# Performance work log

Measured on AMD Instinct MI355X. Metric: run time of the kernel, lower is better.

Reference implementation:

```python
import jax, jax.numpy as jnp
import numpy as np

N, IN_DIM, HID, OUT = 100000, 256, 256, 128
E = 500000


def setup_inputs() -> dict:
    key = jax.random.key(0)
    ks = jax.random.split(key, 12)
    s_in = 1.0 / np.sqrt(IN_DIM)
    s_h = 1.0 / np.sqrt(HID)
    s_c = 1.0 / np.sqrt(2 * OUT)
    return {
        "x": jax.random.normal(ks[0], (N, IN_DIM), dtype=jnp.float32),
        "pos_u": jax.random.randint(ks[1], (E,), 0, N),
        "pos_v": jax.random.randint(ks[2], (E,), 0, N),
        "neg_u": jax.random.randint(ks[3], (E,), 0, N),
        "neg_v": jax.random.randint(ks[4], (E,), 0, N),
        "Wn1": jax.random.normal(ks[5], (IN_DIM, HID), dtype=jnp.float32) * s_in,
        "bn1": jnp.zeros((HID,), dtype=jnp.float32),
        "Wn2": jax.random.normal(ks[6], (HID, OUT), dtype=jnp.float32) * s_h,
        "bn2": jnp.zeros((OUT,), dtype=jnp.float32),
        "Ws1": jax.random.normal(ks[7], (2 * OUT, HID), dtype=jnp.float32) * s_c,
        "bs1": jnp.zeros((HID,), dtype=jnp.float32),
        "Ws2": jax.random.normal(ks[8], (HID, 1), dtype=jnp.float32) * s_h,
        "bs2": jnp.zeros((1,), dtype=jnp.float32),
    }


def _pair_logits(H, u, v, Ws1, bs1, Ws2, bs2):
    hu = H[u]  # [E, OUT] gather
    hv = H[v]
    feats = jnp.concatenate([jnp.abs(hu - hv), hu * hv], axis=-1)  # [E, 2*OUT]
    h = jax.nn.relu(feats @ Ws1 + bs1)
    return (h @ Ws2 + bs2)[..., 0]  # [E]


def reference(x, pos_u, pos_v, neg_u, neg_v,
              Wn1, bn1, Wn2, bn2, Ws1, bs1, Ws2, bs2):
    # node encoder MLP (dropout = identity in eval)
    H = jax.nn.relu(x @ Wn1 + bn1) @ Wn2 + bn2  # [N, OUT]
    pos_logit = _pair_logits(H, pos_u, pos_v, Ws1, bs1, Ws2, bs2)
    neg_logit = _pair_logits(H, neg_u, neg_v, Ws1, bs1, Ws2, bs2)
    return (pos_logit, neg_logit, H)
```

## Files before the change

kernel.cpp:

```cpp
#include <hip/hip_runtime.h>

typedef unsigned short u16;
typedef __bf16 bf16x8 __attribute__((ext_vector_type(8)));
typedef float f32x4 __attribute__((ext_vector_type(4)));
typedef unsigned int u32x4 __attribute__((ext_vector_type(4)));

#define MFMA16(a, b, c) __builtin_amdgcn_mfma_f32_16x16x32_bf16((a), (b), (c), 0, 0, 0)

#define NNODE 100000
#define EDGES 500000
#define NPAIR 1000000

__device__ __forceinline__ u16 bf16bits(float f) {
  __bf16 h = (__bf16)f;
  return __builtin_bit_cast(unsigned short, h);
}

__global__ void prep_weights(const float* __restrict__ Wn1,
                             const float* __restrict__ Wn2,
                             const float* __restrict__ Ws1,
                             u16* __restrict__ ws) {
  int gid = blockIdx.x * 256 + threadIdx.x;
  const float* src;
  int ldn;
  u16* dst;
  int e;
  if (gid < 65536) {
    src = Wn1; ldn = 256; dst = ws; e = gid;
  } else if (gid < 98304) {
    src = Wn2; ldn = 128; dst = ws + 65536; e = gid - 65536;
  } else {
    src = Ws1; ldn = 256; dst = ws + 98304; e = gid - 98304;
  }
  int j = e & 7;
  int lane = (e >> 3) & 63;
  int s = (e >> 9) & 7;
  int nt = e >> 12;
  int n = (nt << 4) | (lane & 15);
  int k = (s << 5) | (((lane >> 4) & 3) << 3) | j;
  dst[e] = bf16bits(src[k * ldn + n]);
}

__launch_bounds__(256, 2)
__global__ void node_kernel(const float* __restrict__ x,
                            const u16* __restrict__ WnT1,
                            const u16* __restrict__ WnT2,
                            const float* __restrict__ bn1,
                            const float* __restrict__ bn2,
                            float* __restrict__ Hout) {
  __shared__ __align__(16) u16 buf[32768];
  const int tid = threadIdx.x;
  const int w = tid >> 6, l = tid & 63;
  const int lg = l >> 4, ll = l & 15;
  const int rowbase = blockIdx.x * 128 + w * 32;

  bf16x8 af[2][8];
#pragma unroll
  for (int m = 0; m < 2; m++) {
    int r = rowbase + m * 16 + ll;
    if (r > NNODE - 1) r = NNODE - 1;
    const float* xp = x + (long)r * 256 + lg * 8;
#pragma unroll
    for (int c = 0; c < 8; c++) {
      f32x4 a0 = *(const f32x4*)(xp + c * 32);
      f32x4 a1 = *(const f32x4*)(xp + c * 32 + 4);
      bf16x8 d;
#pragma unroll
      for (int j = 0; j < 4; j++) {
        d[j] = (__bf16)a0[j];
        d[j + 4] = (__bf16)a1[j];
      }
      af[m][c] = d;
    }
  }

  f32x4 acc[2][16];
#pragma unroll
  for (int nh = 0; nh < 2; nh++) {
    if (nh) __syncthreads();
    {
      const u32x4* src = (const u32x4*)(WnT1 + nh * 32768);
      u32x4* dstv = (u32x4*)buf;
#pragma unroll
      for (int i = 0; i < 16; i++) dstv[tid + i * 256] = src[tid + i * 256];
    }
    __syncthreads();
#pragma unroll
    for (int nt = 0; nt < 8; nt++) {
      int n = nh * 128 + nt * 16 + ll;
      float bv = bn1[n];
      f32x4 a0 = {bv, bv, bv, bv}, a1 = a0;
      const u16* bp = buf + nt * 4096 + l * 8;
#pragma unroll
      for (int s = 0; s < 8; s++) {
        bf16x8 bw = *(const bf16x8*)(bp + s * 512);
        a0 = MFMA16(af[0][s], bw, a0);
        a1 = MFMA16(af[1][s], bw, a1);
      }
      acc[0][nh * 8 + nt] = a0;
      acc[1][nh * 8 + nt] = a1;
    }
  }
  __syncthreads();

  const int hbase = w * 8192;
#pragma unroll
  for (int m = 0; m < 2; m++) {
#pragma unroll
    for (int q = 0; q < 16; q++) {
      int s2 = q >> 1;
      int k3 = ((q & 1) << 1) | (ll >> 3);
      int j = ll & 7;
      f32x4 a = acc[m][q];
#pragma unroll
      for (int t = 0; t < 4; t++) {
        int lane2 = k3 * 16 + lg * 4 + t;
        buf[hbase + ((m * 8 + s2) * 64 + lane2) * 8 + j] = bf16bits(fmaxf(a[t], 0.f));
      }
    }
  }

#pragma unroll
  for (int m = 0; m < 2; m++) {
#pragma unroll
    for (int s = 0; s < 8; s++) {
      af[m][s] = *(const bf16x8*)(buf + hbase + ((m * 8 + s) * 64 + l) * 8);
    }
  }

#pragma unroll
  for (int nt = 0; nt < 8; nt++) {
    int n = nt * 16 + ll;
    float bv = bn2[n];
    f32x4 a0 = {bv, bv, bv, bv}, a1 = a0;
    const u16* bp = WnT2 + nt * 4096 + l * 8;
#pragma unroll
    for (int s = 0; s < 8; s++) {
      bf16x8 bw = *(const bf16x8*)(bp + s * 512);
      a0 = MFMA16(af[0][s], bw, a0);
      a1 = MFMA16(af[1][s], bw, a1);
    }
#pragma unroll
    for (int t = 0; t < 4; t++) {
      int r0 = rowbase + lg * 4 + t;
      if (r0 < NNODE) Hout[(long)r0 * 128 + n] = a0[t];
      int r1 = rowbase + 16 + lg * 4 + t;
      if (r1 < NNODE) Hout[(long)r1 * 128 + n] = a1[t];
    }
  }
}

__launch_bounds__(256, 2)
__global__ void pair_kernel(const float* __restrict__ H,
                            const int* __restrict__ pos_u,
                            const int* __restrict__ pos_v,
                            const int* __restrict__ neg_u,
                            const int* __restrict__ neg_v,
                            const u16* __restrict__ WsT,
                            const float* __restrict__ bs1,
                            const float* __restrict__ Ws2,
                            const float* __restrict__ bs2,
                            float* __restrict__ out) {
  __shared__ __align__(16) u16 buf[32768];
  const int tid = threadIdx.x;
  const int w = tid >> 6, l = tid & 63;
  const int lg = l >> 4, ll = l & 15;
  const int base = blockIdx.x * 128 + w * 32;

  bf16x8 af[2][8];
#pragma unroll
  for (int m = 0; m < 2; m++) {
    int p = base + m * 16 + ll;
    int pe = (p < NPAIR) ? p : 0;
    int u, v;
    if (pe < EDGES) {
      u = pos_u[pe];
      v = pos_v[pe];
    } else {
      u = neg_u[pe - EDGES];
      v = neg_v[pe - EDGES];
    }
    const float* hu = H + (long)u * 128 + lg * 8;
    const float* hv = H + (long)v * 128 + lg * 8;
#pragma unroll
    for (int c = 0; c < 4; c++) {
      f32x4 a0 = *(const f32x4*)(hu + c * 32);
      f32x4 a1 = *(const f32x4*)(hu + c * 32 + 4);
      f32x4 b0 = *(const f32x4*)(hv + c * 32);
      f32x4 b1 = *(const f32x4*)(hv + c * 32 + 4);
      bf16x8 d, pr;
#pragma unroll
      for (int j = 0; j < 4; j++) {
        d[j] = (__bf16)__builtin_fabsf(a0[j] - b0[j]);
        d[j + 4] = (__bf16)__builtin_fabsf(a1[j] - b1[j]);
        pr[j] = (__bf16)(a0[j] * b0[j]);
        pr[j + 4] = (__bf16)(a1[j] * b1[j]);
      }
      af[m][c] = d;
      af[m][c + 4] = pr;
    }
  }

  float lp[2][4] = {{0.f, 0.f, 0.f, 0.f}, {0.f, 0.f, 0.f, 0.f}};
#pragma unroll
  for (int nh = 0; nh < 2; nh++) {
    if (nh) __syncthreads();
    {
      const u32x4* src = (const u32x4*)(WsT + nh * 32768);
      u32x4* dstv = (u32x4*)buf;
#pragma unroll
      for (int i = 0; i < 16; i++) dstv[tid + i * 256] = src[tid + i * 256];
    }
    __syncthreads();
#pragma unroll
    for (int nt = 0; nt < 8; nt++) {
      int n = nh * 128 + nt * 16 + ll;
      float bv = bs1[n];
      f32x4 acc0 = {bv, bv, bv, bv}, acc1 = acc0;
      const u16* bp = buf + nt * 4096 + l * 8;
#pragma unroll
      for (int s = 0; s < 8; s++) {
        bf16x8 bw = *(const bf16x8*)(bp + s * 512);
        acc0 = MFMA16(af[0][s], bw, acc0);
        acc1 = MFMA16(af[1][s], bw, acc1);
      }
      float w2 = Ws2[n];
#pragma unroll
      for (int t = 0; t < 4; t++) {
        lp[0][t] += fmaxf(acc0[t], 0.f) * w2;
        lp[1][t] += fmaxf(acc1[t], 0.f) * w2;
      }
    }
  }

  float b2 = bs2[0];
#pragma unroll
  for (int m = 0; m < 2; m++) {
#pragma unroll
    for (int t = 0; t < 4; t++) {
      float v = lp[m][t];
      v += __shfl_xor(v, 1, 16);
      v += __shfl_xor(v, 2, 16);
      v += __shfl_xor(v, 4, 16);
      v += __shfl_xor(v, 8, 16);
      if (ll == 0) {
        int p = base + m * 16 + lg * 4 + t;
        if (p < NPAIR) out[p] = v + b2;
      }
    }
  }
}

extern "C" void kernel_launch(void* const* d_in, const int* in_sizes, int n_in,
                              void* d_out, int out_size, void* d_ws, size_t ws_size,
                              hipStream_t stream) {
  (void)in_sizes; (void)n_in; (void)out_size; (void)ws_size;
  const float* x = (const float*)d_in[0];
  const int* pos_u = (const int*)d_in[1];
  const int* pos_v = (const int*)d_in[2];
  const int* neg_u = (const int*)d_in[3];
  const int* neg_v = (const int*)d_in[4];
  const float* Wn1 = (const float*)d_in[5];
  const float* bn1 = (const float*)d_in[6];
  const float* Wn2 = (const float*)d_in[7];
  const float* bn2 = (const float*)d_in[8];
  const float* Ws1 = (const float*)d_in[9];
  const float* bs1 = (const float*)d_in[10];
  const float* Ws2 = (const float*)d_in[11];
  const float* bs2 = (const float*)d_in[12];
  float* out = (float*)d_out;
  u16* wsp = (u16*)d_ws;

  float* Hout = out + NPAIR;

  prep_weights<<<640, 256, 0, stream>>>(Wn1, Wn2, Ws1, wsp);
  node_kernel<<<(NNODE + 127) / 128, 256, 0, stream>>>(x, wsp, wsp + 65536, bn1, bn2, Hout);
  pair_kernel<<<(NPAIR + 127) / 128, 256, 0, stream>>>(Hout, pos_u, pos_v, neg_u, neg_v,
                                                       wsp + 98304, bs1, Ws2, bs2, out);
}
```

Baseline: 306.9 us.

## Gather bf16 node embeddings in persistent pair kernel with LDS-resident weights

Node kernel additionally writes a bf16 copy of H into workspace, and a new persistent pair kernel gathers from it, halving gather bytes and doing diff/product in packed bf16. The pair kernel loads all Ws1 into 128KB LDS once per block, keeps biases and Ws2 in registers, and processes 64 pairs per wave in a grid-stride loop. This removes per-block weight reloads but lowers occupancy and slightly changes numerics; the bf16 path depends on workspace size.

Result: slower. 1.113 ms (+262.8%).

```diff
diff --git a/kernel.cpp b/kernel.cpp
--- a/kernel.cpp
+++ b/kernel.cpp
@@ -47,7 +47,8 @@
                             const u16* __restrict__ WnT2,
                             const float* __restrict__ bn1,
                             const float* __restrict__ bn2,
-                            float* __restrict__ Hout) {
+                            float* __restrict__ Hout,
+                            u16* __restrict__ Hb) {
   __shared__ __align__(16) u16 buf[32768];
   const int tid = threadIdx.x;
   const int w = tid >> 6, l = tid & 63;
@@ -143,109 +144,132 @@
 #pragma unroll
     for (int t = 0; t < 4; t++) {
       int r0 = rowbase + lg * 4 + t;
-      if (r0 < NNODE) Hout[(long)r0 * 128 + n] = a0[t];
+      if (r0 < NNODE) {
+        Hout[(long)r0 * 128 + n] = a0[t];
+        if (Hb) Hb[(long)r0 * 128 + n] = bf16bits(a0[t]);
+      }
       int r1 = rowbase + 16 + lg * 4 + t;
-      if (r1 < NNODE) Hout[(long)r1 * 128 + n] = a1[t];
-    }
-  }
-}
-
-__launch_bounds__(256, 2)
-__global__ void pair_kernel(const float* __restrict__ H,
-                            const int* __restrict__ pos_u,
-                            const int* __restrict__ pos_v,
-                            const int* __restrict__ neg_u,
-                            const int* __restrict__ neg_v,
-                            const u16* __restrict__ WsT,
-                            const float* __restrict__ bs1,
-                            const float* __restrict__ Ws2,
-                            const float* __restrict__ bs2,
-                            float* __restrict__ out) {
-  __shared__ __align__(16) u16 buf[32768];
+      if (r1 < NNODE) {
+        Hout[(long)r1 * 128 + n] = a1[t];
+        if (Hb) Hb[(long)r1 * 128 + n] = bf16bits(a1[t]);
+      }
+    }
+  }
+}
+
+template <bool BF16H>
+__launch_bounds__(512, 2)
+__global__ void pair_kernel2(const void* __restrict__ Hsrc,
+                             const int* __restrict__ pos_u,
+                             const int* __restrict__ pos_v,
+                             const int* __restrict__ neg_u,
+                             const int* __restrict__ neg_v,
+                             const u16* __restrict__ WsT,
+                             const float* __restrict__ bs1,
+                             const float* __restrict__ Ws2,
+                             const float* __restrict__ bs2,
+                             float* __restrict__ out) {
+  __shared__ __align__(16) u16 buf[65536];
   const int tid = threadIdx.x;
+  {
+    const u32x4* src = (const u32x4*)WsT;
+    u32x4* dstv = (u32x4*)buf;
+#pragma unroll
+    for (int i = 0; i < 16; i++) dstv[tid + i * 512] = src[tid + i * 512];
+  }
+  __syncthreads();
+
   const int w = tid >> 6, l = tid & 63;
   const int lg = l >> 4, ll = l & 15;
-  const int base = blockIdx.x * 128 + w * 32;
-
-  bf16x8 af[2][8];
-#pragma unroll
-  for (int m = 0; m < 2; m++) {
-    int p = base + m * 16 + ll;
-    int pe = (p < NPAIR) ? p : 0;
-    int u, v;
-    if (pe < EDGES) {
-      u = pos_u[pe];
-      v = pos_v[pe];
-    } else {
-      u = neg_u[pe - EDGES];
-      v = neg_v[pe - EDGES];
-    }
-    const float* hu = H + (long)u * 128 + lg * 8;
-    const float* hv = H + (long)v * 128 + lg * 8;
-#pragma unroll
-    for (int c = 0; c < 4; c++) {
-      f32x4 a0 = *(const f32x4*)(hu + c * 32);
-      f32x4 a1 = *(const f32x4*)(hu + c * 32 + 4);
-      f32x4 b0 = *(const f32x4*)(hv + c * 32);
-      f32x4 b1 = *(const f32x4*)(hv + c * 32 + 4);
-      bf16x8 d, pr;
-#pragma unroll
-      for (int j = 0; j < 4; j++) {
-        d[j] = (__bf16)__builtin_fabsf(a0[j] - b0[j]);
-        d[j + 4] = (__bf16)__builtin_fabsf(a1[j] - b1[j]);
-        pr[j] = (__bf16)(a0[j] * b0[j]);
-        pr[j + 4] = (__bf16)(a1[j] * b1[j]);
-      }
-      af[m][c] = d;
-      af[m][c + 4] = pr;
-    }
-  }
-
-  float lp[2][4] = {{0.f, 0.f, 0.f, 0.f}, {0.f, 0.f, 0.f, 0.f}};
-#pragma unroll
-  for (int nh = 0; nh < 2; nh++) {
-    if (nh) __syncthreads();
-    {
-      const u32x4* src = (const u32x4*)(WsT + nh * 32768);
-      u32x4* dstv = (u32x4*)buf;
-#pragma unroll
-      for (int i = 0; i < 16; i++) dstv[tid + i * 256] = src[tid + i * 256];
-    }
-    __syncthreads();
-#pragma unroll
-    for (int nt = 0; nt < 8; nt++) {
-      int n = nh * 128 + nt * 16 + ll;
-      float bv = bs1[n];
-      f32x4 acc0 = {bv, bv, bv, bv}, acc1 = acc0;
+
+  float w2v[16], b1v[16];
+#pragma unroll
+  for (int nt = 0; nt < 16; nt++) {
+    w2v[nt] = Ws2[nt * 16 + ll];
+    b1v[nt] = bs1[nt * 16 + ll];
+  }
+  const float b2 = bs2[0];
+
+  const int nwaves = gridDim.x * 8;
+  for (int tile = blockIdx.x * 8 + w; tile < 15625; tile += nwaves) {
+    const int base = tile * 64;
+
+    bf16x8 af[4][8];
+#pragma unroll
+    for (int m = 0; m < 4; m++) {
+      int p = base + m * 16 + ll;
+      bool pos = p < EDGES;
+      int idx = pos ? p : p - EDGES;
+      const int* ul = pos ? pos_u : neg_u;
+      const int* vl = pos ? pos_v : neg_v;
+      int u = ul[idx];
+      int v = vl[idx];
+      if constexpr (BF16H) {
+        const u16* hu = (const u16*)Hsrc + (long)u * 128 + lg * 8;
+        const u16* hv = (const u16*)Hsrc + (long)v * 128 + lg * 8;
+#pragma unroll
+        for (int c = 0; c < 4; c++) {
+          bf16x8 a = *(const bf16x8*)(hu + c * 32);
+          bf16x8 b = *(const bf16x8*)(hv + c * 32);
+          bf16x8 d = a - b;
+          u32x4 du = __builtin_bit_cast(u32x4, d) & 0x7FFF7FFFu;
+          af[m][c] = __builtin_bit_cast(bf16x8, du);
+          af[m][c + 4] = a * b;
+        }
+      } else {
+        const float* hu = (const float*)Hsrc + (long)u * 128 + lg * 8;
+        const float* hv = (const float*)Hsrc + (long)v * 128 + lg * 8;
+#pragma unroll
+        for (int c = 0; c < 4; c++) {
+          f32x4 a0 = *(const f32x4*)(hu + c * 32);
+          f32x4 a1 = *(const f32x4*)(hu + c * 32 + 4);
+          f32x4 b0 = *(const f32x4*)(hv + c * 32);
+          f32x4 b1 = *(const f32x4*)(hv + c * 32 + 4);
+          bf16x8 d, pr;
+#pragma unroll
+          for (int j = 0; j < 4; j++) {
+            d[j] = (__bf16)__builtin_fabsf(a0[j] - b0[j]);
+            d[j + 4] = (__bf16)__builtin_fabsf(a1[j] - b1[j]);
+            pr[j] = (__bf16)(a0[j] * b0[j]);
+            pr[j + 4] = (__bf16)(a1[j] * b1[j]);
+          }
+          af[m][c] = d;
+          af[m][c + 4] = pr;
+        }
+      }
+    }
+
+    float lp[4][4] = {};
+#pragma unroll
+    for (int nt = 0; nt < 16; nt++) {
+      float bv = b1v[nt];
+      f32x4 acc[4];
+#pragma unroll
+      for (int m = 0; m < 4; m++) acc[m] = (f32x4){bv, bv, bv, bv};
       const u16* bp = buf + nt * 4096 + l * 8;
 #pragma unroll
       for (int s = 0; s < 8; s++) {
         bf16x8 bw = *(const bf16x8*)(bp + s * 512);
-        acc0 = MFMA16(af[0][s], bw, acc0);
-        acc1 = MFMA16(af[1][s], bw, acc1);
-      }
-      float w2 = Ws2[n];
+#pragma unroll
+        for (int m = 0; m < 4; m++) acc[m] = MFMA16(af[m][s], bw, acc[m]);
+      }
+      float w2 = w2v[nt];
+#pragma unroll
+      for (int m = 0; m < 4; m++)
+#pragma unroll
+        for (int t = 0; t < 4; t++) lp[m][t] += fmaxf(acc[m][t], 0.f) * w2;
+    }
+
+#pragma unroll
+    for (int m = 0; m < 4; m++) {
 #pragma unroll
       for (int t = 0; t < 4; t++) {
-        lp[0][t] += fmaxf(acc0[t], 0.f) * w2;
-        lp[1][t] += fmaxf(acc1[t], 0.f) * w2;
-      }
-    }
-  }
-
-  float b2 = bs2[0];
-#pragma unroll
-  for (int m = 0; m < 2; m++) {
-#pragma unroll
-    for (int t = 0; t < 4; t++) {
-      float v = lp[m][t];
-      v += __shfl_xor(v, 1, 16);
-      v += __shfl_xor(v, 2, 16);
-      v += __shfl_xor(v, 4, 16);
-      v += __shfl_xor(v, 8, 16);
-      if (ll == 0) {
-        int p = base + m * 16 + lg * 4 + t;
-        if (p < NPAIR) out[p] = v + b2;
+        float v = lp[m][t];
+        v += __shfl_xor(v, 1, 16);
+        v += __shfl_xor(v, 2, 16);
+        v += __shfl_xor(v, 4, 16);
+        v += __shfl_xor(v, 8, 16);
+        if (ll == 0) out[base + m * 16 + lg * 4 + t] = v + b2;
       }
     }
   }
@@ -254,7 +278,7 @@
 extern "C" void kernel_launch(void* const* d_in, const int* in_sizes, int n_in,
                               void* d_out, int out_size, void* d_ws, size_t ws_size,
                               hipStream_t stream) {
-  (void)in_sizes; (void)n_in; (void)out_size; (void)ws_size;
+  (void)in_sizes; (void)n_in; (void)out_size;
   const float* x = (const float*)d_in[0];
   const int* pos_u = (const int*)d_in[1];
   const int* pos_v = (const int*)d_in[2];
@@ -272,9 +296,18 @@
   u16* wsp = (u16*)d_ws;
 
   float* Hout = out + NPAIR;
+  const size_t need = 327680 + (size_t)NNODE * 128 * 2;
+  const bool bf16h = ws_size >= need;
+  u16* Hb = bf16h ? (wsp + 163840) : nullptr;
 
   prep_weights<<<640, 256, 0, stream>>>(Wn1, Wn2, Ws1, wsp);
-  node_kernel<<<(NNODE + 127) / 128, 256, 0, stream>>>(x, wsp, wsp + 65536, bn1, bn2, Hout);
-  pair_kernel<<<(NPAIR + 127) / 128, 256, 0, stream>>>(Hout, pos_u, pos_v, neg_u, neg_v,
-                                                       wsp + 98304, bs1, Ws2, bs2, out);
-}
+  node_kernel<<<(NNODE + 127) / 128, 256, 0, stream>>>(x, wsp, wsp + 65536, bn1, bn2,
+                                                       Hout, Hb);
+  if (bf16h) {
+    pair_kernel2<true><<<256, 512, 0, stream>>>(Hb, pos_u, pos_v, neg_u, neg_v,
+                                                wsp + 98304, bs1, Ws2, bs2, out);
+  } else {
+    pair_kernel2<false><<<256, 512, 0, stream>>>(Hout, pos_u, pos_v, neg_u, neg_v,
+                                                 wsp + 98304, bs1, Ws2, bs2, out);
+  }
+}
```
